# Optimization experiments

Hardware: AMD Instinct MI355X
Metric: run time of the kernel (lower is better)

The kernel has to match this reference:

```python
import jax, jax.numpy as jnp
import numpy as np

IN_DIM, OUT_DIM, K, NUM = 512, 512, 3, 16
BATCH = 256


def setup_inputs() -> dict:
    key = jax.random.key(0)
    k1, k2 = jax.random.split(key, 2)
    x = jax.random.normal(k1, (BATCH, IN_DIM), dtype=jnp.float32)
    # uniform grid on [-1,1] extended by K knots each side (extend_grid)
    h = 2.0 / NUM
    g1d = jnp.arange(-K, NUM + K + 1, dtype=jnp.float32) * h - 1.0  # (NUM+1+2K,)
    grid = jnp.tile(g1d[None, :], (IN_DIM, 1))  # (in_dim, 24)
    coef = jax.random.normal(k2, (IN_DIM, OUT_DIM, NUM + K), dtype=jnp.float32) * 0.1
    scale_sp = jnp.ones((IN_DIM, OUT_DIM), jnp.float32) * (1.0 / np.sqrt(IN_DIM).astype(np.float32))
    mask = jnp.ones((IN_DIM, OUT_DIM), jnp.float32)
    return {"x": x, "grid": grid, "coef": coef, "scale_sp": scale_sp, "mask": mask}


def b_spline_basis(x, grid, k):
    # x: (B, I); grid: (I, G).  Cox-de Boor recursion, vectorized.
    xg = x[:, :, None]          # (B, I, 1)
    g = grid[None, :, :]        # (1, I, G)
    B = ((xg >= g[:, :, :-1]) & (xg < g[:, :, 1:])).astype(x.dtype)  # order-0
    for kk in range(1, k + 1):
        B = ((xg - g[:, :, :-(kk + 1)]) / (g[:, :, kk:-1] - g[:, :, :-(kk + 1)]) * B[:, :, :-1]
             + (g[:, :, kk + 1:] - xg) / (g[:, :, kk + 1:] - g[:, :, 1:-kk]) * B[:, :, 1:])
    return B  # (B, I, NUM + K)


def reference(x, grid, coef, scale_sp, mask):
    base = jax.nn.silu(x)                              # (B, I) base_fun branch
    Bmat = b_spline_basis(x, grid, K)                  # (B, I, NUM+K)
    y = jnp.einsum('big,iog->bio', Bmat, coef)         # coef2curve -> (B, I, O)
    y = (base[:, :, None] + scale_sp[None, :, :] * y) * mask[None, :, :]
    return jnp.sum(y, axis=1)                          # (B, O)
```

## Files before the change

kernel.cpp:

```cpp
#include <hip/hip_runtime.h>

#define IN_DIM   512
#define OUT_DIM  512
#define KDEG     3
#define BATCH    256
#define NB       19
#define NG       23
#define KAUG     20
#define KTOT     (IN_DIM * KAUG)

typedef short  bf16x8 __attribute__((ext_vector_type(8)));
typedef float  f32x4  __attribute__((ext_vector_type(4)));

__device__ __forceinline__ unsigned short f2bf(float f) {
    union { float f; unsigned int u; } v; v.f = f;
    unsigned int r = (v.u + 0x7FFF + ((v.u >> 16) & 1)) >> 16;
    return (unsigned short)r;
}

__device__ __forceinline__ void async_copy16(const void* gsrc, const void* ldst) {
    auto g = (const __attribute__((address_space(1))) unsigned int*)((unsigned long long)gsrc);
    auto l = (__attribute__((address_space(3))) unsigned int*)((unsigned int)(unsigned long long)ldst);
    __builtin_amdgcn_global_load_lds(g, l, 16, 0, 0);
}

__global__ void build_A(const float* __restrict__ X,
                        const float* __restrict__ G,
                        unsigned short* __restrict__ A) {
    int t = blockIdx.x * blockDim.x + threadIdx.x;
    if (t >= BATCH * IN_DIM) return;
    int b = t / IN_DIM;
    int i = t - b * IN_DIM;

    float x = X[t];

    float gr[NG];
    const float* g = G + i * NG;
#pragma unroll
    for (int j = 0; j < NG; j++) gr[j] = g[j];

    float B[NG - 1];
#pragma unroll
    for (int j = 0; j < NG - 1; j++)
        B[j] = (x >= gr[j] && x < gr[j + 1]) ? 1.0f : 0.0f;

#pragma unroll
    for (int kk = 1; kk <= KDEG; kk++) {
#pragma unroll
        for (int j = 0; j < NG - 1 - kk; j++) {
            float d1 = gr[j + kk] - gr[j];
            float d2 = gr[j + kk + 1] - gr[j + 1];
            B[j] = (x - gr[j]) / d1 * B[j] +
                   (gr[j + kk + 1] - x) / d2 * B[j + 1];
        }
    }

    unsigned short v[KAUG];
#pragma unroll
    for (int j = 0; j < NB; j++) v[j] = f2bf(B[j]);
    v[NB] = f2bf(x / (1.0f + __expf(-x)));

    unsigned int* dst = (unsigned int*)(A + (size_t)b * KTOT + i * KAUG);
    const unsigned int* src = (const unsigned int*)v;
#pragma unroll
    for (int d = 0; d < KAUG / 2; d++) dst[d] = src[d];
}

__global__ void build_Wt(const float* __restrict__ coef,
                         const float* __restrict__ scale_sp,
                         const float* __restrict__ mask,
                         unsigned short* __restrict__ Wt) {
    int t = blockIdx.x * blockDim.x + threadIdx.x;
    int i = t >> 9;
    int o = t & 511;
    int io = i * OUT_DIM + o;
    float m  = mask[io];
    float sm = scale_sp[io] * m;
    const float* c = coef + (size_t)io * NB;

    unsigned short v[KAUG];
#pragma unroll
    for (int g = 0; g < NB; g++) v[g] = f2bf(c[g] * sm);
    v[NB] = f2bf(m);

    unsigned int* dst = (unsigned int*)(Wt + (size_t)o * KTOT + i * KAUG);
    const unsigned int* src = (const unsigned int*)v;
#pragma unroll
    for (int d = 0; d < KAUG / 2; d++) dst[d] = src[d];
}

#define BM 128
#define BN 64
#define BK 32
#define SPLITS 16
#define KCH (KTOT / SPLITS)

__global__ __launch_bounds__(256) void gemm_mfma(const unsigned short* __restrict__ A,
                                                 const unsigned short* __restrict__ Wt,
                                                 float* __restrict__ out) {
    __shared__ __align__(16) unsigned short As[BM * BK];
    __shared__ __align__(16) unsigned short Bs[BN * BK];

    int tid  = threadIdx.x;
    int lane = tid & 63;
    int w    = tid >> 6;
    int wm   = w >> 1;
    int wn   = w & 1;
    int m0 = blockIdx.y * BM;
    int n0 = blockIdx.x * BN;
    int kbase = blockIdx.z * KCH;

    const unsigned short* Ablk = A  + (size_t)m0 * KTOT + kbase;
    const unsigned short* Bblk = Wt + (size_t)n0 * KTOT + kbase;

    f32x4 acc[4][2];
#pragma unroll
    for (int i = 0; i < 4; i++)
#pragma unroll
        for (int j = 0; j < 2; j++) acc[i][j] = (f32x4)0.0f;

    int quad = lane >> 4;
    int lr   = lane & 15;

    for (int kk = 0; kk < KCH; kk += BK) {
        {
            int s = w * 64 + lane;
            async_copy16(Ablk + (size_t)(s >> 2) * KTOT + kk + (s & 3) * 8,
                         (const char*)As + (w * 64) * 16);
            s = 256 + w * 64 + lane;
            async_copy16(Ablk + (size_t)(s >> 2) * KTOT + kk + (s & 3) * 8,
                         (const char*)As + (256 + w * 64) * 16);
        }
        {
            int s = w * 64 + lane;
            async_copy16(Bblk + (size_t)(s >> 2) * KTOT + kk + (s & 3) * 8,
                         (const char*)Bs + (w * 64) * 16);
        }
        __syncthreads();

        bf16x8 af[4], bfg[2];
#pragma unroll
        for (int mt = 0; mt < 4; mt++)
            af[mt] = *(const bf16x8*)&As[(wm * 64 + mt * 16 + lr) * BK + quad * 8];
#pragma unroll
        for (int nt = 0; nt < 2; nt++)
            bfg[nt] = *(const bf16x8*)&Bs[(wn * 32 + nt * 16 + lr) * BK + quad * 8];

#pragma unroll
        for (int mt = 0; mt < 4; mt++)
#pragma unroll
            for (int nt = 0; nt < 2; nt++)
                acc[mt][nt] = __builtin_amdgcn_mfma_f32_16x16x32_bf16(
                    af[mt], bfg[nt], acc[mt][nt], 0, 0, 0);

        __syncthreads();
    }

#pragma unroll
    for (int mt = 0; mt < 4; mt++) {
#pragma unroll
        for (int nt = 0; nt < 2; nt++) {
            int col = n0 + wn * 32 + nt * 16 + lr;
            int rb  = m0 + wm * 64 + mt * 16 + quad * 4;
#pragma unroll
            for (int r = 0; r < 4; r++)
                atomicAdd(&out[(size_t)(rb + r) * OUT_DIM + col], acc[mt][nt][r]);
        }
    }
}

extern "C" void kernel_launch(void* const* d_in, const int* in_sizes, int n_in,
                              void* d_out, int out_size, void* d_ws, size_t ws_size,
                              hipStream_t stream) {
    const float* x        = (const float*)d_in[0];
    const float* grid     = (const float*)d_in[1];
    const float* coef     = (const float*)d_in[2];
    const float* scale_sp = (const float*)d_in[3];
    const float* mask     = (const float*)d_in[4];
    float* out = (float*)d_out;

    unsigned short* A  = (unsigned short*)d_ws;
    unsigned short* Wt = A + (size_t)BATCH * KTOT;

    build_A<<<dim3((BATCH * IN_DIM + 255) / 256), dim3(256), 0, stream>>>(x, grid, A);
    build_Wt<<<dim3((IN_DIM * OUT_DIM) / 256), dim3(256), 0, stream>>>(coef, scale_sp, mask, Wt);

    hipMemsetAsync(d_out, 0, (size_t)out_size * sizeof(float), stream);
    gemm_mfma<<<dim3(OUT_DIM / BN, BATCH / BM, SPLITS), dim3(256), 0, stream>>>(A, Wt, out);
}
```

Measured before the change: 110.9 us.

## Fuse weight packing into GEMM and stream A directly from global memory

Removes the separate build_Wt kernel and its bf16 workspace by converting each block's coef/scale/mask slice into a padded LDS tile inside the GEMM. The GEMM now covers all 256 batch rows per block, with 8 waves each reading their A fragments straight from global memory, and no staging loop or per-step barriers. This saves one launch and a write-plus-read of the packed weight matrix. In exchange, A loads go uncached-in-LDS with strided row accesses, and each block reads 32 KB of coef fp32 before it can start computing.

After: 101.5 us. 1.09x faster.

```diff
diff --git a/kernel.cpp b/kernel.cpp
--- a/kernel.cpp
+++ b/kernel.cpp
@@ -16,12 +16,6 @@
     union { float f; unsigned int u; } v; v.f = f;
     unsigned int r = (v.u + 0x7FFF + ((v.u >> 16) & 1)) >> 16;
     return (unsigned short)r;
-}
-
-__device__ __forceinline__ void async_copy16(const void* gsrc, const void* ldst) {
-    auto g = (const __attribute__((address_space(1))) unsigned int*)((unsigned long long)gsrc);
-    auto l = (__attribute__((address_space(3))) unsigned int*)((unsigned int)(unsigned long long)ldst);
-    __builtin_amdgcn_global_load_lds(g, l, 16, 0, 0);
 }
 
 __global__ void build_A(const float* __restrict__ X,
@@ -66,102 +60,81 @@
     for (int d = 0; d < KAUG / 2; d++) dst[d] = src[d];
 }
 
-__global__ void build_Wt(const float* __restrict__ coef,
-                         const float* __restrict__ scale_sp,
-                         const float* __restrict__ mask,
-                         unsigned short* __restrict__ Wt) {
-    int t = blockIdx.x * blockDim.x + threadIdx.x;
-    int i = t >> 9;
-    int o = t & 511;
-    int io = i * OUT_DIM + o;
-    float m  = mask[io];
-    float sm = scale_sp[io] * m;
-    const float* c = coef + (size_t)io * NB;
+#define BN     32
+#define SPLITS 16
+#define ICH    32
+#define KCH    (ICH * KAUG)
+#define LDS_K  (KCH + 8)
 
-    unsigned short v[KAUG];
+__global__ __launch_bounds__(512) void gemm_fused(const unsigned short* __restrict__ A,
+                                                  const float* __restrict__ coef,
+                                                  const float* __restrict__ scale_sp,
+                                                  const float* __restrict__ mask,
+                                                  float* __restrict__ out) {
+    __shared__ __align__(16) unsigned short Bs[BN * LDS_K];
+
+    int tid = threadIdx.x;
+    int o0 = blockIdx.x * BN;
+    int i0 = blockIdx.z * ICH;
+    int kbase = blockIdx.z * KCH;
+
 #pragma unroll
-    for (int g = 0; g < NB; g++) v[g] = f2bf(c[g] * sm);
-    v[NB] = f2bf(m);
+    for (int s = 0; s < 2; s++) {
+        int p = tid + s * 512;
+        int o = p & 31;
+        int di = p >> 5;
+        int io = (i0 + di) * OUT_DIM + (o0 + o);
+        float m  = mask[io];
+        float sm = scale_sp[io] * m;
+        const float* c = coef + (size_t)io * NB;
 
-    unsigned int* dst = (unsigned int*)(Wt + (size_t)o * KTOT + i * KAUG);
-    const unsigned int* src = (const unsigned int*)v;
+        __align__(8) unsigned short v[KAUG];
 #pragma unroll
-    for (int d = 0; d < KAUG / 2; d++) dst[d] = src[d];
-}
+        for (int g = 0; g < NB; g++) v[g] = f2bf(c[g] * sm);
+        v[NB] = f2bf(m);
 
-#define BM 128
-#define BN 64
-#define BK 32
-#define SPLITS 16
-#define KCH (KTOT / SPLITS)
+        unsigned long long* dst =
+            (unsigned long long*)((char*)Bs + (size_t)o * (LDS_K * 2) + di * (KAUG * 2));
+        const unsigned long long* src = (const unsigned long long*)v;
+#pragma unroll
+        for (int d = 0; d < 5; d++) dst[d] = src[d];
+    }
+    __syncthreads();
 
-__global__ __launch_bounds__(256) void gemm_mfma(const unsigned short* __restrict__ A,
-                                                 const unsigned short* __restrict__ Wt,
-                                                 float* __restrict__ out) {
-    __shared__ __align__(16) unsigned short As[BM * BK];
-    __shared__ __align__(16) unsigned short Bs[BN * BK];
-
-    int tid  = threadIdx.x;
     int lane = tid & 63;
     int w    = tid >> 6;
-    int wm   = w >> 1;
-    int wn   = w & 1;
-    int m0 = blockIdx.y * BM;
-    int n0 = blockIdx.x * BN;
-    int kbase = blockIdx.z * KCH;
+    int quad = lane >> 4;
+    int lr   = lane & 15;
 
-    const unsigned short* Ablk = A  + (size_t)m0 * KTOT + kbase;
-    const unsigned short* Bblk = Wt + (size_t)n0 * KTOT + kbase;
-
-    f32x4 acc[4][2];
+    f32x4 acc[2][2];
 #pragma unroll
-    for (int i = 0; i < 4; i++)
+    for (int i = 0; i < 2; i++)
 #pragma unroll
         for (int j = 0; j < 2; j++) acc[i][j] = (f32x4)0.0f;
 
-    int quad = lane >> 4;
-    int lr   = lane & 15;
-
-    for (int kk = 0; kk < KCH; kk += BK) {
-        {
-            int s = w * 64 + lane;
-            async_copy16(Ablk + (size_t)(s >> 2) * KTOT + kk + (s & 3) * 8,
-                         (const char*)As + (w * 64) * 16);
-            s = 256 + w * 64 + lane;
-            async_copy16(Ablk + (size_t)(s >> 2) * KTOT + kk + (s & 3) * 8,
-                         (const char*)As + (256 + w * 64) * 16);
-        }
-        {
-            int s = w * 64 + lane;
-            async_copy16(Bblk + (size_t)(s >> 2) * KTOT + kk + (s & 3) * 8,
-                         (const char*)Bs + (w * 64) * 16);
-        }
-        __syncthreads();
-
-        bf16x8 af[4], bfg[2];
-#pragma unroll
-        for (int mt = 0; mt < 4; mt++)
-            af[mt] = *(const bf16x8*)&As[(wm * 64 + mt * 16 + lr) * BK + quad * 8];
-#pragma unroll
-        for (int nt = 0; nt < 2; nt++)
-            bfg[nt] = *(const bf16x8*)&Bs[(wn * 32 + nt * 16 + lr) * BK + quad * 8];
+    const unsigned short* a0 = A + (size_t)(w * 32 + lr)      * KTOT + kbase + quad * 8;
+    const unsigned short* a1 = A + (size_t)(w * 32 + 16 + lr) * KTOT + kbase + quad * 8;
+    const unsigned short* b0 = &Bs[(size_t)lr        * LDS_K + quad * 8];
+    const unsigned short* b1 = &Bs[(size_t)(16 + lr) * LDS_K + quad * 8];
 
 #pragma unroll
-        for (int mt = 0; mt < 4; mt++)
-#pragma unroll
-            for (int nt = 0; nt < 2; nt++)
-                acc[mt][nt] = __builtin_amdgcn_mfma_f32_16x16x32_bf16(
-                    af[mt], bfg[nt], acc[mt][nt], 0, 0, 0);
-
-        __syncthreads();
+    for (int kk = 0; kk < KCH; kk += 32) {
+        bf16x8 af0 = *(const bf16x8*)(a0 + kk);
+        bf16x8 af1 = *(const bf16x8*)(a1 + kk);
+        bf16x8 bf0 = *(const bf16x8*)(b0 + kk);
+        bf16x8 bf1 = *(const bf16x8*)(b1 + kk);
+        acc[0][0] = __builtin_amdgcn_mfma_f32_16x16x32_bf16(af0, bf0, acc[0][0], 0, 0, 0);
+        acc[0][1] = __builtin_amdgcn_mfma_f32_16x16x32_bf16(af0, bf1, acc[0][1], 0, 0, 0);
+        acc[1][0] = __builtin_amdgcn_mfma_f32_16x16x32_bf16(af1, bf0, acc[1][0], 0, 0, 0);
+        acc[1][1] = __builtin_amdgcn_mfma_f32_16x16x32_bf16(af1, bf1, acc[1][1], 0, 0, 0);
     }
 
 #pragma unroll
-    for (int mt = 0; mt < 4; mt++) {
+    for (int mt = 0; mt < 2; mt++) {
 #pragma unroll
         for (int nt = 0; nt < 2; nt++) {
-            int col = n0 + wn * 32 + nt * 16 + lr;
-            int rb  = m0 + wm * 64 + mt * 16 + quad * 4;
+            int col = o0 + nt * 16 + lr;
+            int rb  = w * 32 + mt * 16 + quad * 4;
 #pragma unroll
             for (int r = 0; r < 4; r++)
                 atomicAdd(&out[(size_t)(rb + r) * OUT_DIM + col], acc[mt][nt][r]);
@@ -179,12 +152,11 @@
     const float* mask     = (const float*)d_in[4];
     float* out = (float*)d_out;
 
-    unsigned short* A  = (unsigned short*)d_ws;
-    unsigned short* Wt = A + (size_t)BATCH * KTOT;
+    unsigned short* A = (unsigned short*)d_ws;
 
     build_A<<<dim3((BATCH * IN_DIM + 255) / 256), dim3(256), 0, stream>>>(x, grid, A);
-    build_Wt<<<dim3((IN_DIM * OUT_DIM) / 256), dim3(256), 0, stream>>>(coef, scale_sp, mask, Wt);
 
     hipMemsetAsync(d_out, 0, (size_t)out_size * sizeof(float), stream);
-    gemm_mfma<<<dim3(OUT_DIM / BN, BATCH / BM, SPLITS), dim3(256), 0, stream>>>(A, Wt, out);
+    gemm_fused<<<dim3(OUT_DIM / BN, 1, SPLITS), dim3(512), 0, stream>>>(
+        A, coef, scale_sp, mask, out);
 }
```
